# Kernel optimization log

Hardware: AMD Instinct MI355X
Metric: run time of the kernel (lower is better)

Reference implementation:

```python
import jax, jax.numpy as jnp
import numpy as np

N_NODES = 50000
N_EDGES = 800000
D_IN = 64
D_OUT = 64


def setup_inputs() -> dict:
    key = jax.random.key(0)
    ks = jax.random.split(key, 5)
    feat = jax.random.normal(ks[0], (N_NODES, D_IN), dtype=jnp.float32)
    src = jax.random.randint(ks[1], (N_EDGES,), 0, N_NODES, dtype=jnp.int64)
    dst = jax.random.randint(ks[2], (N_EDGES,), 0, N_NODES, dtype=jnp.int64)
    # Xavier-uniform-ish scale for weights
    lim = float(np.sqrt(6.0 / (D_IN + D_OUT)) * np.sqrt(2.0))
    W_neigh = jax.random.uniform(ks[3], (D_OUT, D_IN), dtype=jnp.float32, minval=-lim, maxval=lim)
    W_self = jax.random.uniform(ks[4], (D_OUT, D_IN), dtype=jnp.float32, minval=-lim, maxval=lim)
    b_self = jnp.zeros((D_OUT,), dtype=jnp.float32)
    return {"feat": feat, "src": src, "dst": dst,
            "W_neigh": W_neigh, "W_self": W_self, "b_self": b_self}


def reference(feat, src, dst, W_neigh, W_self, b_self):
    # srcdata = fc_neigh(feat_src)  -> [N, D_OUT]
    srcdata = feat @ W_neigh.T
    # A_div.T @ srcdata == mean of transformed source feats over in-edges per dst.
    # deg[j] = A.sum(0)[j]; column scaling by 1/deg then transpose-SpMM.
    agg = jax.ops.segment_sum(srcdata[src], dst, num_segments=N_NODES)  # [N, D_OUT]
    deg = jax.ops.segment_sum(jnp.ones_like(dst, dtype=srcdata.dtype), dst,
                              num_segments=N_NODES)  # [N]
    # Zero-degree columns stay zero in the sparse product (no stored nonzeros).
    dstdata = jnp.where(deg[:, None] > 0, agg / jnp.maximum(deg, 1.0)[:, None], 0.0)
    # rst = fc_self(feat_dst) + dstdata ; feat_dst = feat[:N_dst] = feat (square A)
    return feat @ W_self.T + b_self + dstdata
```

## Files before the change

### kernel.cpp

```cpp
#include <hip/hip_runtime.h>

#define N_NODES 50000
#define N_EDGES 800000
#define D 64
#define RB 64
#define NBUCK 782
#define CHUNK 2048
#define NCHUNK 391
#define SUBCAP 24
#define NFEATBLK 3125
#define SCAP 1280
#define ALD 68

typedef __attribute__((ext_vector_type(8))) __bf16 bf16x8;
typedef __attribute__((ext_vector_type(4))) float f32x4;
typedef __attribute__((ext_vector_type(2))) float f32x2;

__device__ inline unsigned f2bf(float f) {
    unsigned b = __builtin_bit_cast(unsigned, f);
    b += 0x7fffu + ((b >> 16) & 1u);
    return b >> 16;
}

__device__ inline void acc16p(f32x2* a, uint4 v) {
    a[0] += __builtin_amdgcn_cvt_pk_f32_fp8((int)v.x, false);
    a[1] += __builtin_amdgcn_cvt_pk_f32_fp8((int)v.x, true);
    a[2] += __builtin_amdgcn_cvt_pk_f32_fp8((int)v.y, false);
    a[3] += __builtin_amdgcn_cvt_pk_f32_fp8((int)v.y, true);
    a[4] += __builtin_amdgcn_cvt_pk_f32_fp8((int)v.z, false);
    a[5] += __builtin_amdgcn_cvt_pk_f32_fp8((int)v.z, true);
    a[6] += __builtin_amdgcn_cvt_pk_f32_fp8((int)v.w, false);
    a[7] += __builtin_amdgcn_cvt_pk_f32_fp8((int)v.w, true);
}

__global__ __launch_bounds__(256) void prep_scatter_kernel(
        const float* __restrict__ feat, const float* __restrict__ Wn, const float* __restrict__ Ws,
        const int* __restrict__ src, const int* __restrict__ dst,
        unsigned* __restrict__ fq,
        unsigned short* __restrict__ wnb, unsigned short* __restrict__ wsb,
        unsigned int* __restrict__ ebuf, unsigned char* __restrict__ cntArr) {
    __shared__ int cntB[NBUCK];
    int b = blockIdx.x;
    int t = threadIdx.x;
    if (b < NCHUNK) {
        for (int i = t; i < NBUCK; i += 256) cntB[i] = 0;
        __syncthreads();
        int e0 = b * CHUNK;
#pragma unroll
        for (int k = 0; k < 8; ++k) {
            int e = e0 + k * 256 + t;
            if (e < N_EDGES) {
                int dv = dst[e];
                int bk = dv >> 6;
                int slot = atomicAdd(&cntB[bk], 1);
                if (slot < SUBCAP)
                    ebuf[((size_t)bk * NCHUNK + b) * SUBCAP + slot] =
                        (unsigned)src[e] | ((unsigned)(dv & (RB - 1)) << 16);
            }
        }
        __syncthreads();
        for (int i = t; i < NBUCK; i += 256) {
            int c = cntB[i];
            cntArr[(size_t)b * NBUCK + i] = (unsigned char)(c < SUBCAP ? c : SUBCAP);
        }
    } else if (b < NCHUNK + NFEATBLK) {
        int i = (b - NCHUNK) * 256 + t;
        float4 v = ((const float4*)feat)[i];
        int q = __builtin_amdgcn_cvt_pk_fp8_f32(v.x, v.y, 0, false);
        q = __builtin_amdgcn_cvt_pk_fp8_f32(v.z, v.w, q, true);
        fq[i] = (unsigned)q;
    } else {
        for (int i = t; i < D * D; i += 256) {
            wnb[i] = (unsigned short)f2bf(Wn[i]);
            wsb[i] = (unsigned short)f2bf(Ws[i]);
        }
    }
}

__global__ __launch_bounds__(256) void gather_mfma_kernel(
        const float* __restrict__ feat, const unsigned char* __restrict__ fq,
        const unsigned int* __restrict__ ebuf, const unsigned char* __restrict__ cntArr,
        const unsigned short* __restrict__ wsb, const unsigned short* __restrict__ wnb,
        const float* __restrict__ bias, float* __restrict__ out) {
    __shared__ int cnt[RB];
    __shared__ int cur[RB];
    __shared__ unsigned short sorted[SCAP];
    __shared__ float agg[RB * ALD];
    int t = threadIdx.x;
    int bk = blockIdx.x;
    if (t < RB) cnt[t] = 0;
    __syncthreads();
    for (int c = t; c < NCHUNK; c += 256) {
        int cc = cntArr[(size_t)c * NBUCK + bk];
        const unsigned int* slab = ebuf + ((size_t)bk * NCHUNK + c) * SUBCAP;
        for (int j = 0; j < cc; j += 4) {
            uint4 v = *(const uint4*)(slab + j);
            atomicAdd(&cnt[(v.x >> 16) & (RB - 1)], 1);
            if (j + 1 < cc) atomicAdd(&cnt[(v.y >> 16) & (RB - 1)], 1);
            if (j + 2 < cc) atomicAdd(&cnt[(v.z >> 16) & (RB - 1)], 1);
            if (j + 3 < cc) atomicAdd(&cnt[(v.w >> 16) & (RB - 1)], 1);
        }
    }
    __syncthreads();
    if (t < RB) {
        int c = cnt[t];
        int s = c;
#pragma unroll
        for (int d = 1; d < RB; d <<= 1) {
            int v = __shfl_up(s, d, 64);
            if (t >= d) s += v;
        }
        cur[t] = s - c;
    }
    __syncthreads();
    for (int c = t; c < NCHUNK; c += 256) {
        int cc = cntArr[(size_t)c * NBUCK + bk];
        const unsigned int* slab = ebuf + ((size_t)bk * NCHUNK + c) * SUBCAP;
        for (int j = 0; j < cc; j += 4) {
            uint4 v = *(const uint4*)(slab + j);
            int p;
            p = atomicAdd(&cur[(v.x >> 16) & (RB - 1)], 1);
            if (p < SCAP) sorted[p] = (unsigned short)(v.x & 0xFFFFu);
            if (j + 1 < cc) { p = atomicAdd(&cur[(v.y >> 16) & (RB - 1)], 1); if (p < SCAP) sorted[p] = (unsigned short)(v.y & 0xFFFFu); }
            if (j + 2 < cc) { p = atomicAdd(&cur[(v.z >> 16) & (RB - 1)], 1); if (p < SCAP) sorted[p] = (unsigned short)(v.z & 0xFFFFu); }
            if (j + 3 < cc) { p = atomicAdd(&cur[(v.w >> 16) & (RB - 1)], 1); if (p < SCAP) sorted[p] = (unsigned short)(v.w & 0xFFFFu); }
        }
    }
    __syncthreads();
    int ns = t >> 2, p = t & 3;
    int dg = cnt[ns];
    int start = cur[ns] - dg;
    int dgc = dg;
    if (start + dgc > SCAP) dgc = (start < SCAP) ? (SCAP - start) : 0;
    f32x2 acc2[8];
#pragma unroll
    for (int j = 0; j < 8; ++j) acc2[j] = (f32x2){0.f, 0.f};
    const unsigned char* fqp = fq + p * 16;
    int i = 0;
    for (; i + 4 <= dgc; i += 4) {
        int id0 = sorted[start + i + 0];
        int id1 = sorted[start + i + 1];
        int id2 = sorted[start + i + 2];
        int id3 = sorted[start + i + 3];
        uint4 v0 = *(const uint4*)(fqp + (size_t)id0 * D);
        uint4 v1 = *(const uint4*)(fqp + (size_t)id1 * D);
        uint4 v2 = *(const uint4*)(fqp + (size_t)id2 * D);
        uint4 v3 = *(const uint4*)(fqp + (size_t)id3 * D);
        acc16p(acc2, v0); acc16p(acc2, v1); acc16p(acc2, v2); acc16p(acc2, v3);
    }
    for (; i < dgc; ++i) {
        int id = sorted[start + i];
        uint4 v = *(const uint4*)(fqp + (size_t)id * D);
        acc16p(acc2, v);
    }
    float inv = (dg > 0) ? 1.0f / (float)dg : 0.f;
    float* ap = &agg[ns * ALD + p * 16];
#pragma unroll
    for (int j = 0; j < 4; ++j) {
        float4 o = make_float4(acc2[2 * j].x * inv, acc2[2 * j].y * inv,
                               acc2[2 * j + 1].x * inv, acc2[2 * j + 1].y * inv);
        *(float4*)(ap + 4 * j) = o;
    }
    __syncthreads();
    int r0 = blockIdx.x * RB;
    int w = t >> 6, lane = t & 63;
    int m = lane & 15, quad = lane >> 4;
    int row = r0 + 16 * w + m;
    int rowA = row < N_NODES ? row : N_NODES - 1;
    const float* fr = feat + (size_t)rowA * D + quad * 8;
    float4 f0 = *(const float4*)(fr + 0);
    float4 f1 = *(const float4*)(fr + 4);
    float4 f2 = *(const float4*)(fr + 32);
    float4 f3 = *(const float4*)(fr + 36);
    bf16x8 aS0, aS1, aA0, aA1;
    aS0[0] = (__bf16)f0.x; aS0[1] = (__bf16)f0.y; aS0[2] = (__bf16)f0.z; aS0[3] = (__bf16)f0.w;
    aS0[4] = (__bf16)f1.x; aS0[5] = (__bf16)f1.y; aS0[6] = (__bf16)f1.z; aS0[7] = (__bf16)f1.w;
    aS1[0] = (__bf16)f2.x; aS1[1] = (__bf16)f2.y; aS1[2] = (__bf16)f2.z; aS1[3] = (__bf16)f2.w;
    aS1[4] = (__bf16)f3.x; aS1[5] = (__bf16)f3.y; aS1[6] = (__bf16)f3.z; aS1[7] = (__bf16)f3.w;
#pragma unroll
    for (int j = 0; j < 8; ++j) {
        aA0[j] = (__bf16)agg[(16 * w + m) * ALD + 0  + quad * 8 + j];
        aA1[j] = (__bf16)agg[(16 * w + m) * ALD + 32 + quad * 8 + j];
    }
#pragma unroll
    for (int tt = 0; tt < 4; ++tt) {
        int nn = 16 * tt + m;
        bf16x8 bS0 = *(const bf16x8*)(wsb + (size_t)nn * D + 0  + quad * 8);
        bf16x8 bS1 = *(const bf16x8*)(wsb + (size_t)nn * D + 32 + quad * 8);
        bf16x8 bN0 = *(const bf16x8*)(wnb + (size_t)nn * D + 0  + quad * 8);
        bf16x8 bN1 = *(const bf16x8*)(wnb + (size_t)nn * D + 32 + quad * 8);
        f32x4 cc4 = {0.f, 0.f, 0.f, 0.f};
        cc4 = __builtin_amdgcn_mfma_f32_16x16x32_bf16(aS0, bS0, cc4, 0, 0, 0);
        cc4 = __builtin_amdgcn_mfma_f32_16x16x32_bf16(aS1, bS1, cc4, 0, 0, 0);
        cc4 = __builtin_amdgcn_mfma_f32_16x16x32_bf16(aA0, bN0, cc4, 0, 0, 0);
        cc4 = __builtin_amdgcn_mfma_f32_16x16x32_bf16(aA1, bN1, cc4, 0, 0, 0);
        float bv = bias[16 * tt + m];
#pragma unroll
        for (int reg = 0; reg < 4; ++reg) {
            int orow = r0 + 16 * w + quad * 4 + reg;
            if (orow < N_NODES)
                out[(size_t)orow * D + 16 * tt + m] = cc4[reg] + bv;
        }
    }
}

extern "C" void kernel_launch(void* const* d_in, const int* in_sizes, int n_in,
                              void* d_out, int out_size, void* d_ws, size_t ws_size,
                              hipStream_t stream) {
    const float* feat  = (const float*)d_in[0];
    const int*   src   = (const int*)d_in[1];
    const int*   dst   = (const int*)d_in[2];
    const float* Wn    = (const float*)d_in[3];
    const float* Wself = (const float*)d_in[4];
    const float* bself = (const float*)d_in[5];
    float* out = (float*)d_out;

    unsigned*       featq = (unsigned*)d_ws;
    unsigned short* wnb   = (unsigned short*)(featq + (size_t)N_NODES * D / 4);
    unsigned short* wsb   = wnb + D * D;
    unsigned int*   ebuf  = (unsigned int*)(wsb + D * D);
    unsigned char*  cntArr = (unsigned char*)(ebuf + (size_t)NBUCK * NCHUNK * SUBCAP);

    prep_scatter_kernel<<<NCHUNK + NFEATBLK + 1, 256, 0, stream>>>(
        feat, Wn, Wself, src, dst, featq, wnb, wsb, ebuf, cntArr);
    gather_mfma_kernel<<<NBUCK, 256, 0, stream>>>(
        feat, (const unsigned char*)featq, ebuf, cntArr, wsb, wnb, bself, out);
}
```

Baseline: 113.8 us.

## Stage bucket edges into shared memory once and enlarge edge chunks

The gather kernel now copies each bucket's edge entries from the global per-chunk slabs into shared memory once, reusing the aggregation buffer. The counting and sorting passes then run over that compact list using all 256 threads, instead of each thread reading the global slabs twice in serial per-chunk loops. The edge chunk size is raised to 8192, with per-chunk capacity raised to 40, so there are fewer chunks and smaller count arrays. The cost is a larger scatter loop per block with fewer scatter blocks, and an extra barrier because the staging area aliases the aggregation buffer.

Result: slower. 122.6 us (+7.7%).

```diff
diff --git a/kernel.cpp b/kernel.cpp
--- a/kernel.cpp
+++ b/kernel.cpp
@@ -5,9 +5,9 @@
 #define D 64
 #define RB 64
 #define NBUCK 782
-#define CHUNK 2048
-#define NCHUNK 391
-#define SUBCAP 24
+#define CHUNK 8192
+#define NCHUNK 98
+#define SUBCAP 40
 #define NFEATBLK 3125
 #define SCAP 1280
 #define ALD 68
@@ -46,8 +46,8 @@
         for (int i = t; i < NBUCK; i += 256) cntB[i] = 0;
         __syncthreads();
         int e0 = b * CHUNK;
-#pragma unroll
-        for (int k = 0; k < 8; ++k) {
+#pragma unroll 4
+        for (int k = 0; k < 32; ++k) {
             int e = e0 + k * 256 + t;
             if (e < N_EDGES) {
                 int dv = dst[e];
@@ -84,23 +84,31 @@
         const float* __restrict__ bias, float* __restrict__ out) {
     __shared__ int cnt[RB];
     __shared__ int cur[RB];
+    __shared__ int tot;
     __shared__ unsigned short sorted[SCAP];
     __shared__ float agg[RB * ALD];
+    unsigned* raw = (unsigned*)agg;
     int t = threadIdx.x;
     int bk = blockIdx.x;
     if (t < RB) cnt[t] = 0;
-    __syncthreads();
-    for (int c = t; c < NCHUNK; c += 256) {
-        int cc = cntArr[(size_t)c * NBUCK + bk];
-        const unsigned int* slab = ebuf + ((size_t)bk * NCHUNK + c) * SUBCAP;
+    if (t == 0) tot = 0;
+    __syncthreads();
+    if (t < NCHUNK) {
+        int cc = cntArr[(size_t)t * NBUCK + bk];
+        int base = atomicAdd(&tot, cc);
+        const unsigned int* slab = ebuf + ((size_t)bk * NCHUNK + t) * SUBCAP;
         for (int j = 0; j < cc; j += 4) {
             uint4 v = *(const uint4*)(slab + j);
-            atomicAdd(&cnt[(v.x >> 16) & (RB - 1)], 1);
-            if (j + 1 < cc) atomicAdd(&cnt[(v.y >> 16) & (RB - 1)], 1);
-            if (j + 2 < cc) atomicAdd(&cnt[(v.z >> 16) & (RB - 1)], 1);
-            if (j + 3 < cc) atomicAdd(&cnt[(v.w >> 16) & (RB - 1)], 1);
-        }
-    }
+            raw[base + j] = v.x;
+            if (j + 1 < cc) raw[base + j + 1] = v.y;
+            if (j + 2 < cc) raw[base + j + 2] = v.z;
+            if (j + 3 < cc) raw[base + j + 3] = v.w;
+        }
+    }
+    __syncthreads();
+    int T = tot;
+    for (int i = t; i < T; i += 256)
+        atomicAdd(&cnt[(raw[i] >> 16) & (RB - 1)], 1);
     __syncthreads();
     if (t < RB) {
         int c = cnt[t];
@@ -113,18 +121,10 @@
         cur[t] = s - c;
     }
     __syncthreads();
-    for (int c = t; c < NCHUNK; c += 256) {
-        int cc = cntArr[(size_t)c * NBUCK + bk];
-        const unsigned int* slab = ebuf + ((size_t)bk * NCHUNK + c) * SUBCAP;
-        for (int j = 0; j < cc; j += 4) {
-            uint4 v = *(const uint4*)(slab + j);
-            int p;
-            p = atomicAdd(&cur[(v.x >> 16) & (RB - 1)], 1);
-            if (p < SCAP) sorted[p] = (unsigned short)(v.x & 0xFFFFu);
-            if (j + 1 < cc) { p = atomicAdd(&cur[(v.y >> 16) & (RB - 1)], 1); if (p < SCAP) sorted[p] = (unsigned short)(v.y & 0xFFFFu); }
-            if (j + 2 < cc) { p = atomicAdd(&cur[(v.z >> 16) & (RB - 1)], 1); if (p < SCAP) sorted[p] = (unsigned short)(v.z & 0xFFFFu); }
-            if (j + 3 < cc) { p = atomicAdd(&cur[(v.w >> 16) & (RB - 1)], 1); if (p < SCAP) sorted[p] = (unsigned short)(v.w & 0xFFFFu); }
-        }
+    for (int i = t; i < T; i += 256) {
+        unsigned r = raw[i];
+        int p = atomicAdd(&cur[(r >> 16) & (RB - 1)], 1);
+        if (p < SCAP) sorted[p] = (unsigned short)(r & 0xFFFFu);
     }
     __syncthreads();
     int ns = t >> 2, p = t & 3;
@@ -153,6 +153,7 @@
         uint4 v = *(const uint4*)(fqp + (size_t)id * D);
         acc16p(acc2, v);
     }
+    __syncthreads();
     float inv = (dg > 0) ? 1.0f / (float)dg : 0.f;
     float* ap = &agg[ns * ALD + p * 16];
 #pragma unroll
```
